# Performance work log

Measured on AMD Instinct MI355X. Metric: run time of the kernel, lower is better.

The kernel has to match this reference:

```python
import jax, jax.numpy as jnp
import numpy as np

D = 256       # dim
M = 50        # num_celltypes
NPATH = 65536 # path tokens (256*256)
N = M + NPATH
FF = 3        # focusing_factor
K = 5         # dwc kernel size


def find_closest_factors(num):
    for i in range(int(num ** 0.5), 0, -1):
        if num % i == 0:
            return (i, num // i)
    return (1, num)


def setup_inputs() -> dict:
    key = jax.random.key(0)
    ks = jax.random.split(key, 16)
    def w(k, shape, s=0.02):
        return jax.random.normal(k, shape, dtype=jnp.float32) * s
    z = lambda *s: jnp.zeros(s, jnp.float32)
    return {
        "x": jax.random.normal(ks[0], (1, N, D), dtype=jnp.float32),
        "W_qkv": w(ks[1], (D, 3 * D)),
        "scale_linear": w(ks[2], (1, 1, D)),
        "dwc_w": w(ks[3], (D, 1, K, K)),
        "dwc_b": w(ks[4], (D,)),
        "Wa": w(ks[5], (D, D)), "ba": z(D),
        "Wb": w(ks[6], (D, D)), "bb": z(D),
        "Wc": w(ks[7], (D, 1)), "bc": z(1),
        "W1": w(ks[8], (D, D)), "b1": z(D),
        "W2": w(ks[9], (D, D)), "b2": z(D),
        "W3a": w(ks[10], (2 * D, D)), "b3a": z(D),
        "W3b": w(ks[11], (D, D)), "b3b": z(D),
        "Wf": w(ks[12], (D, D)), "bf": z(D),
    }


def reference(x, W_qkv, scale_linear, dwc_w, dwc_b, Wa, ba, Wb, bb, Wc, bc,
              W1, b1, W2, b2, W3a, b3a, W3b, b3b, Wf, bf):
    scale = D ** -0.5
    qkv = x @ W_qkv                         # (1, N, 3D)
    q, k, v = jnp.split(qkv, 3, axis=-1)
    qc, qp = q[:, :M], q[:, M:]
    kc, kp = k[:, :M], k[:, M:]
    vc, vp = v[:, :M], v[:, M:]

    # --- softmax attention branches ---
    sa = jax.nn.softmax(jnp.einsum('bic,bjc->bij', qc * scale, kc), axis=-1)
    out_self_celltypes = sa @ vc            # (1, M, D)
    cap = jax.nn.softmax(jnp.einsum('bic,bjc->bij', qp * scale, kc), axis=-1)
    out_cross_path = cap @ vc               # (1, NPATH, D)
    cac = jax.nn.softmax(jnp.einsum('bic,bjc->bij', qc * scale, kp), axis=-1)
    out_cross_celltypes = cac @ vp          # (1, M, D)

    # --- focused linear attention on path tokens ---
    sp = jax.nn.softplus(scale_linear)
    ql = (jax.nn.relu(qp) + 1e-6) / sp
    kl = (jax.nn.relu(kp) + 1e-6) / sp
    qn = jnp.linalg.norm(ql, axis=-1, keepdims=True)
    kn = jnp.linalg.norm(kl, axis=-1, keepdims=True)
    ql = ql ** FF
    kl = kl ** FF
    ql = ql / jnp.linalg.norm(ql, axis=-1, keepdims=True) * qn
    kl = kl / jnp.linalg.norm(kl, axis=-1, keepdims=True) * kn
    zfac = 1.0 / (jnp.einsum('bic,bc->bi', ql, kl.sum(axis=1)) + 1e-6)
    kv = jnp.einsum('bjc,bjd->bcd', kl, vp)                 # (1, D, D)
    out_s = jnp.einsum('bic,bcd,bi->bid', ql, kv, zfac)     # (1, NPATH, D)

    # --- depthwise conv feature map ---
    wc, hc = find_closest_factors(NPATH)
    fm = vp.reshape(1, wc, hc, D).transpose(0, 3, 1, 2)     # b c w h
    fm = jax.lax.conv_general_dilated(
        fm, dwc_w, (1, 1), 'SAME',
        dimension_numbers=('NCHW', 'OIHW', 'NCHW'), feature_group_count=D)
    fm = fm + dwc_b[None, :, None, None]
    fm = fm.transpose(0, 2, 3, 1).reshape(1, NPATH, D)
    out_self_path = (out_s + fm) @ Wf + bf  # feamap_linear (dropout=eval)

    # --- gated attention net (shared weights, 4 calls) ---
    def gated(t):
        t = t[0]  # squeeze batch -> (n, D)
        a = jnp.tanh(t @ Wa + ba)
        g = jax.nn.sigmoid(t @ Wb + bb)
        return (a * g) @ Wc + bc  # (n, 1)

    A_cc = gated(out_cross_celltypes)
    A_cp = gated(out_cross_path)
    A_sc = gated(out_self_celltypes)
    A_sp = gated(out_self_path)

    # --- attention fusion (shared weights, 2 calls) ---
    def fuse(A1, A2, x1, x2):
        h1 = jax.nn.softmax(A1.T, axis=1) @ x1[0]   # (1, D)
        h1 = jax.nn.relu(h1 @ W1 + b1)
        h2 = jax.nn.softmax(A2.T, axis=1) @ x2[0]
        h2 = jax.nn.relu(h2 @ W2 + b2)
        f = jnp.concatenate([h1, h2], axis=1)       # (1, 2D)
        return jax.nn.relu(jax.nn.relu(f @ W3a + b3a) @ W3b + b3b)

    fusion_cross = fuse(A_cc, A_cp, out_cross_celltypes, out_cross_path)
    fusion_self = fuse(A_sc, A_sp, out_self_celltypes, out_self_path)
    return jnp.concatenate([fusion_cross, fusion_self], axis=1)  # (1, 2D)
```

## Files before the change

### kernel.cpp

```cpp
#include <hip/hip_runtime.h>
#include <hip/hip_bf16.h>
#include <math.h>


constexpr int DD = 256;
constexpr int MM = 50;
constexpr float SCL = 0.0625f;

constexpr size_t B_VPH = 0;
constexpr size_t B_QLH = (size_t)32 << 20;
constexpr size_t B_KLH = (size_t)64 << 20;
constexpr size_t B_E   = (size_t)96 << 20;
constexpr size_t B_SM  = (size_t)112 << 20;
constexpr size_t B_X   = B_SM + ((size_t)2 << 20);

constexpr size_t KLSUMR = 0;
constexpr size_t KLSUMP = 256;
constexpr size_t OCCDENP= 2304;
constexpr size_t W50P   = 2816;
constexpr size_t EDENP  = 3328;
constexpr size_t H2TP   = 3336;
constexpr size_t H2DENP = 5384;
constexpr size_t OCCRAW = 5392;
constexpr size_t ZEND   = 18192;
constexpr size_t QC     = ZEND;
constexpr size_t KC     = QC + 12800;
constexpr size_t VC     = KC + 12800;
constexpr size_t VCA    = VC + 12800;
constexpr size_t VCB    = VCA + 12800;
constexpr size_t WFA    = VCB + 12800;
constexpr size_t WFB    = WFA + 65536;
constexpr size_t BFA    = WFB + 65536;
constexpr size_t BFB    = BFA + 256;
constexpr size_t OSCB   = BFB + 256;
constexpr size_t OCCB   = OSCB + 12800;
constexpr size_t ASC    = OCCB + 12800;
constexpr size_t ACC50  = ASC + 64;
constexpr size_t SMEND  = ACC50 + 64;

constexpr size_t XT_WQKV = 0;
constexpr size_t XT_WFAT = 196608;
constexpr size_t XT_WFBT = 262144;
constexpr size_t XT_KVT  = 327680;
constexpr size_t XT_QCH  = 393216;
constexpr size_t XT_KCH  = 409600;
constexpr size_t XT_VCAT = 425984;
constexpr size_t XT_VCBT = 442368;
constexpr size_t XT_END  = 458752;
constexpr size_t WS_NEEDED = B_X + XT_END * 2;

typedef short bf16x8 __attribute__((ext_vector_type(8)));
typedef float f32x4 __attribute__((ext_vector_type(4)));

__device__ __forceinline__ float rcpf_(float x){ return __builtin_amdgcn_rcpf(x); }
__device__ __forceinline__ float fsig_(float x){ return rcpf_(1.0f + __expf(-x)); }
__device__ __forceinline__ float ftanh_(float x){ return 1.0f - 2.0f * rcpf_(__expf(2.0f * x) + 1.0f); }

__device__ __forceinline__ float bf2f(unsigned short u){
  return __uint_as_float(((unsigned int)u) << 16);
}
__device__ __forceinline__ unsigned short f2bf(float f){
  union { __hip_bfloat16 h; unsigned short u; } c;
  c.h = __float2bfloat16(f);
  return c.u;
}
__device__ __forceinline__ f32x4 mfma16(bf16x8 a, bf16x8 b, f32x4 c){
  return __builtin_amdgcn_mfma_f32_16x16x32_bf16(a, b, c, 0, 0, 0);
}

__device__ __forceinline__ float waveAllSum(float v){
  #pragma unroll
  for (int m = 1; m < 64; m <<= 1) v += __shfl_xor(v, m, 64);
  return v;
}

__device__ __forceinline__ size_t fragIdx(int n, int k, int K8){
  const int tile = n >> 4, cn = n & 15;
  const int k0 = k >> 5, kqi = (k >> 3) & 3, e = k & 7;
  return (((size_t)tile * K8 + k0) * 64 + (kqi * 16 + cn)) * 8 + e;
}

__device__ __forceinline__ int kvOff(int c, int k){
  return c * 40 + (c >> 3) * 8 + k;
}

__global__ void __launch_bounds__(256) k_prep0(const float* __restrict__ x, const float* __restrict__ Wqkv,
                                               float* qc, float* kc, float* vc,
                                               unsigned short* qch, unsigned short* kch,
                                               unsigned short* __restrict__ WT,
                                               const float* __restrict__ Wa, const float* __restrict__ Wb,
                                               const float* __restrict__ ba, const float* __restrict__ bb,
                                               const float* __restrict__ Wf, const float* __restrict__ bf,
                                               float* Wfa, float* Wfb, float* bfa, float* bfb,
                                               unsigned short* WfaTh, unsigned short* WfbTh){
  const int b = blockIdx.x, t = threadIdx.x;
  if (b < 48) {
    __shared__ unsigned short Tt[64][72];
    const int bn = b % 12, bk = b / 12;
    const int n0 = bn * 64, k0g = bk * 64;
    #pragma unroll
    for (int i = 0; i < 16; i++) {
      const int k_l = (t >> 6) + i * 4;
      const int n_l = t & 63;
      Tt[n_l][k_l] = f2bf(Wqkv[(size_t)(k0g + k_l) * 768 + n0 + n_l]);
    }
    __syncthreads();
    #pragma unroll
    for (int i = 0; i < 2; i++) {
      const int fr = t * 2 + i;
      const int t_l = fr >> 7;
      const int k0_l = (fr >> 6) & 1;
      const int lane_f = fr & 63;
      const int n_l = t_l * 16 + (lane_f & 15);
      const int k_l = k0_l * 32 + (lane_f >> 4) * 8;
      const int tg = (n0 >> 4) + t_l;
      const int k0gl = (k0g >> 5) + k0_l;
      bf16x8 v = *(const bf16x8*)&Tt[n_l][k_l];
      *(bf16x8*)&WT[(((size_t)tg * 8 + k0gl) * 64 + lane_f) * 8] = v;
    }
    return;
  }
  __shared__ float xs[256];
  const int j = t;
  if (b < 98) {
    const int r = b - 48;
    xs[j] = x[r * DD + j];
    __syncthreads();
    float aq = 0.f, ak = 0.f, av = 0.f;
    for (int k = 0; k < DD; k++) {
      float xv = xs[k];
      aq += xv * Wqkv[k * 768 + j];
      ak += xv * Wqkv[k * 768 + 256 + j];
      av += xv * Wqkv[k * 768 + 512 + j];
    }
    qc[r * DD + j] = aq; kc[r * DD + j] = ak; vc[r * DD + j] = av;
    qch[fragIdx(r, j, 8)] = f2bf(aq);
    kch[fragIdx(r, j, 8)] = f2bf(ak);
    if (r == 0) {
      for (int c = 50; c < 64; c++) {
        qch[fragIdx(c, j, 8)] = 0;
        kch[fragIdx(c, j, 8)] = 0;
      }
    }
    return;
  }
  const int bb2 = b - 98;
  const float* src; const float* Wm;
  if (bb2 < 256)      { src = Wf + bb2 * DD;         Wm = Wa; }
  else if (bb2 < 512) { src = Wf + (bb2 - 256) * DD; Wm = Wb; }
  else if (bb2 == 512){ src = bf;                    Wm = Wa; }
  else                { src = bf;                    Wm = Wb; }
  xs[j] = src[j];
  __syncthreads();
  float a = 0.f;
  for (int k = 0; k < DD; k++) a += xs[k] * Wm[k * DD + j];
  if (bb2 < 256)      { Wfa[bb2 * DD + j] = a; WfaTh[fragIdx(j, bb2, 8)] = f2bf(a); }
  else if (bb2 < 512) { Wfb[(bb2 - 256) * DD + j] = a; WfbTh[fragIdx(j, bb2 - 256, 8)] = f2bf(a); }
  else if (bb2 == 512) bfa[j] = a + ba[j];
  else bfb[j] = a + bb[j];
}

__global__ void __launch_bounds__(256) k_prep1(const float* vc, const float* Wa, const float* Wb,
                                               float* Vca, float* Vcb,
                                               unsigned short* VcaTh, unsigned short* VcbTh){
  __shared__ float rs[256];
  const int b = blockIdx.x, j = threadIdx.x;
  const int r = b;
  rs[j] = vc[r * DD + j];
  __syncthreads();
  float a = 0.f, bv = 0.f;
  for (int k = 0; k < DD; k++) { float v = rs[k]; a += v * Wa[k * DD + j]; bv += v * Wb[k * DD + j]; }
  Vca[r * DD + j] = a; Vcb[r * DD + j] = bv;
  VcaTh[fragIdx(j, r, 2)] = f2bf(a);
  VcbTh[fragIdx(j, r, 2)] = f2bf(bv);
  if (r == 0) {
    for (int c = 50; c < 64; c++) {
      VcaTh[fragIdx(j, c, 2)] = 0;
      VcbTh[fragIdx(j, c, 2)] = 0;
    }
  }
}

__global__ void __launch_bounds__(256) k_oscg(const float* __restrict__ qc, const float* __restrict__ kc,
                                              const float* __restrict__ vc,
                                              const float* __restrict__ Wa, const float* __restrict__ Wb,
                                              const float* __restrict__ ba, const float* __restrict__ bb,
                                              const float* __restrict__ Wc, const float* __restrict__ bc,
                                              float* __restrict__ osc, float* __restrict__ A){
  const int i = blockIdx.x, t = threadIdx.x;
  __shared__ float qs[256];
  __shared__ float P[64];
  __shared__ float red[4];
  qs[t] = qc[i * DD + t];
  __syncthreads();
  if (t < 64) {
    float s = -1e30f;
    if (t < 50) {
      float acc = 0.f;
      const float4* kr = (const float4*)&kc[t * DD];
      #pragma unroll 8
      for (int k = 0; k < 64; k++) {
        float4 kv = kr[k];
        float4 qv = *(const float4*)&qs[k * 4];
        acc += qv.x * kv.x + qv.y * kv.y + qv.z * kv.z + qv.w * kv.w;
      }
      s = acc * SCL;
    }
    float mx = s;
    #pragma unroll
    for (int m = 1; m < 64; m <<= 1) mx = fmaxf(mx, __shfl_xor(mx, m, 64));
    float e = (t < 50) ? __expf(s - mx) : 0.f;
    float den = waveAllSum(e);
    P[t] = e * rcpf_(den);
  }
  __syncthreads();
  float a = 0.f;
  for (int jj = 0; jj < 50; jj++) a += P[jj] * vc[jj * DD + t];
  osc[i * DD + t] = a;
  __syncthreads();
  qs[t] = a;
  __syncthreads();
  float u = 0.f, v = 0.f;
  for (int k = 0; k < DD; k++) { float tv = qs[k]; u += tv * Wa[k * DD + t]; v += tv * Wb[k * DD + t]; }
  float g = ftanh_(u + ba[t]) * fsig_(v + bb[t]) * Wc[t];
  g = waveAllSum(g);
  const int lane = t & 63, wv = t >> 6;
  if (lane == 0) red[wv] = g;
  __syncthreads();
  if (t == 0) A[i] = red[0] + red[1] + red[2] + red[3] + bc[0];
}

__global__ void __launch_bounds__(256) k_gated(const float* __restrict__ tin,
                                               const float* __restrict__ Wa, const float* __restrict__ Wb,
                                               const float* __restrict__ ba, const float* __restrict__ bb,
                                               const float* __restrict__ Wc, const float* __restrict__ bc,
                                               float* __restrict__ A){
  int r = blockIdx.x, j = threadIdx.x;
  __shared__ float ts[256];
  __shared__ float red[4];
  ts[j] = tin[r * DD + j];
  __syncthreads();
  float u = 0.f, v = 0.f;
  for (int k = 0; k < DD; k++) { float tv = ts[k]; u += tv * Wa[k * DD + j]; v += tv * Wb[k * DD + j]; }
  float g = ftanh_(u + ba[j]) * fsig_(v + bb[j]) * Wc[j];
  g = waveAllSum(g);
  int lane = j & 63, wv = j >> 6;
  if (lane == 0) red[wv] = g;
  __syncthreads();
  if (j == 0) A[r] = red[0] + red[1] + red[2] + red[3] + bc[0];
}

__global__ void __launch_bounds__(256) k_path1(
    const float* __restrict__ x, const unsigned short* __restrict__ WTf,
    const float* __restrict__ sln,
    const unsigned short* __restrict__ kchf, const unsigned short* __restrict__ qchf,
    const unsigned short* __restrict__ VcaTf, const unsigned short* __restrict__ VcbTf,
    const float* __restrict__ ba, const float* __restrict__ bb,
    const float* __restrict__ Wc, const float* __restrict__ bc,
    unsigned short* __restrict__ vph, unsigned short* __restrict__ qlh, unsigned short* __restrict__ klh,
    unsigned short* __restrict__ Eh, float* __restrict__ w50p, float* __restrict__ edenp, float* __restrict__ occdenp){
  __shared__ __align__(16) char arena[38912];
  unsigned short (*Psh)[72]   = (unsigned short (*)[72])arena;
  float (*denp)[4]            = (float (*)[4])(arena + 4608);
  unsigned short (*qpsb)[264] = (unsigned short (*)[264])(arena + 5120);
  unsigned short (*kpsb)[264] = (unsigned short (*)[264])(arena + 22016);

  const int tid = threadIdx.x;
  const int i0 = blockIdx.x * 32;
  const int part = blockIdx.x & 7;
  const int lane = tid & 63;
  const int wvv = tid >> 6;
  const int cn = lane & 15;
  const int m0 = (lane >> 4) * 4;
  const int kq = (lane >> 4) * 8;

  for (int l = tid; l < 2048; l += 256) {
    const int r = l >> 6, c4 = (l & 63) * 4;
    const float4 xv = *(const float4*)&x[(size_t)(MM + i0 + r) * DD + c4];
    ushort4 o; o.x = f2bf(xv.x); o.y = f2bf(xv.y); o.z = f2bf(xv.z); o.w = f2bf(xv.w);
    *(ushort4*)&qpsb[r][c4] = o;
  }
  __syncthreads();

  bf16x8 af0[8], af1[8];
  #pragma unroll
  for (int k0 = 0; k0 < 8; k0++) {
    af0[k0] = *(const bf16x8*)&qpsb[cn][k0 * 32 + kq];
    af1[k0] = *(const bf16x8*)&qpsb[16 + cn][k0 * 32 + kq];
  }
  __syncthreads();

  bf16x8 b0[8], b1[8];
  {
    const unsigned short* Bt = WTf + ((size_t)wvv * 8 * 64 + lane) * 8;
    #pragma unroll
    for (int k0 = 0; k0 < 8; k0++) b0[k0] = *(const bf16x8*)&Bt[(size_t)k0 * 512];
  }
  #pragma unroll 1
  for (int tt = 0; tt < 12; tt++) {
    const int t = wvv + 4 * tt;
    if (tt + 1 < 12) {
      const unsigned short* Bt = WTf + (((size_t)(t + 4) * 8) * 64 + lane) * 8;
      #pragma unroll
      for (int k0 = 0; k0 < 8; k0++) b1[k0] = *(const bf16x8*)&Bt[(size_t)k0 * 512];
    }
    f32x4 acc0 = {0.f, 0.f, 0.f, 0.f};
    f32x4 acc1 = {0.f, 0.f, 0.f, 0.f};
    #pragma unroll
    for (int k0 = 0; k0 < 8; k0++) {
      acc0 = mfma16(af0[k0], b0[k0], acc0);
      acc1 = mfma16(af1[k0], b0[k0], acc1);
    }
    if (t < 16) {
      int c = t * 16 + cn;
      #pragma unroll
      for (int i = 0; i < 4; i++) {
        qpsb[m0 + i][c] = f2bf(acc0[i]);
        qpsb[16 + m0 + i][c] = f2bf(acc1[i]);
      }
    } else if (t < 32) {
      int c = (t - 16) * 16 + cn;
      #pragma unroll
      for (int i = 0; i < 4; i++) {
        kpsb[m0 + i][c] = f2bf(acc0[i]);
        kpsb[16 + m0 + i][c] = f2bf(acc1[i]);
      }
    } else {
      int c = (t - 32) * 16 + cn;
      #pragma unroll
      for (int i = 0; i < 4; i++) {
        vph[(size_t)(i0 + m0 + i) * DD + c] = f2bf(acc0[i]);
        vph[(size_t)(i0 + 16 + m0 + i) * DD + c] = f2bf(acc1[i]);
      }
    }
    #pragma unroll
    for (int k0 = 0; k0 < 8; k0++) b0[k0] = b1[k0];
  }
  __syncthreads();

  float ep0[4], ep1[4];
  {
    f32x4 accp0 = {0.f,0.f,0.f,0.f}, accp1 = {0.f,0.f,0.f,0.f};
    f32x4 accc0 = {0.f,0.f,0.f,0.f}, accc1 = {0.f,0.f,0.f,0.f};
    const unsigned short* Bk = kchf + ((size_t)wvv * 8 * 64 + lane) * 8;
    const unsigned short* Bq = qchf + ((size_t)wvv * 8 * 64 + lane) * 8;
    #pragma unroll
    for (int k0 = 0; k0 < 8; k0++) {
      bf16x8 aq0 = *(const bf16x8*)&qpsb[cn][k0 * 32 + kq];
      bf16x8 aq1 = *(const bf16x8*)&qpsb[16 + cn][k0 * 32 + kq];
      bf16x8 ak0 = *(const bf16x8*)&kpsb[cn][k0 * 32 + kq];
      bf16x8 ak1 = *(const bf16x8*)&kpsb[16 + cn][k0 * 32 + kq];
      bf16x8 bk = *(const bf16x8*)&Bk[(size_t)k0 * 512];
      bf16x8 bq = *(const bf16x8*)&Bq[(size_t)k0 * 512];
      accp0 = mfma16(aq0, bk, accp0);
      accp1 = mfma16(aq1, bk, accp1);
      accc0 = mfma16(ak0, bq, accc0);
      accc1 = mfma16(ak1, bq, accc1);
    }
    const int col = wvv * 16 + cn;
    const bool ok = (col < 50);
    #pragma unroll
    for (int i = 0; i < 4; i++) {
      ep0[i] = ok ? __expf(accp0[i] * SCL) : 0.f;
      ep1[i] = ok ? __expf(accp1[i] * SCL) : 0.f;
    }
    float osum = 0.f;
    #pragma unroll
    for (int i = 0; i < 4; i++) {
      unsigned short h0 = ok ? f2bf(__expf(accc0[i] * SCL)) : (unsigned short)0;
      unsigned short h1 = ok ? f2bf(__expf(accc1[i] * SCL)) : (unsigned short)0;
      Eh[(size_t)(i0 + m0 + i) * 64 + col] = h0;
      Eh[(size_t)(i0 + 16 + m0 + i) * 64 + col] = h1;
      if (ok) osum += bf2f(h0) + bf2f(h1);
    }
    osum += __shfl_xor(osum, 16, 64);
    osum += __shfl_xor(osum, 32, 64);
    if (lane < 16 && ok) atomicAdd(&occdenp[part * 64 + col], osum);
    float d0[4], d1[4];
    #pragma unroll
    for (int i = 0; i < 4; i++) { d0[i] = ep0[i]; d1[i] = ep1[i]; }
    #pragma unroll
    for (int m = 1; m < 16; m <<= 1) {
      #pragma unroll
      for (int i = 0; i < 4; i++) {
        d0[i] += __shfl_xor(d0[i], m, 64);
        d1[i] += __shfl_xor(d1[i], m, 64);
      }
    }
    if (cn == 0) {
      #pragma unroll
      for (int i = 0; i < 4; i++) {
        denp[m0 + i][wvv] = d0[i];
        denp[16 + m0 + i][wvv] = d1[i];
      }
    }
  }
  __syncthreads();

  {
    const int col = wvv * 16 + cn;
    #pragma unroll
    for (int i = 0; i < 4; i++) {
      float4 dp = *(const float4*)&denp[m0 + i][0];
      Psh[m0 + i][col] = f2bf(ep0[i] * rcpf_(dp.x + dp.y + dp.z + dp.w));
      float4 dq = *(const float4*)&denp[16 + m0 + i][0];
      Psh[16 + m0 + i][col] = f2bf(ep1[i] * rcpf_(dq.x + dq.y + dq.z + dq.w));
    }
  }

  float4 sl4 = ((const float4*)sln)[lane];
  float4 rsp;
  rsp.x = rcpf_(log1pf(expf(sl4.x))); rsp.y = rcpf_(log1pf(expf(sl4.y)));
  rsp.z = rcpf_(log1pf(expf(sl4.z))); rsp.w = rcpf_(log1pf(expf(sl4.w)));
  float4 ba4 = ((const float4*)ba)[lane];
  float4 bb4 = ((const float4*)bb)[lane];
  float4 wc4 = ((const float4*)Wc)[lane];
  float bcv = bc[0];
  for (int rr = 0; rr < 8; rr++) {
    const int r = wvv * 8 + rr;
    const int row = i0 + r;
    ushort4 qu = *(const ushort4*)&qpsb[r][lane * 4];
    ushort4 ku = *(const ushort4*)&kpsb[r][lane * 4];
    float4 q4 = {bf2f(qu.x), bf2f(qu.y), bf2f(qu.z), bf2f(qu.w)};
    float4 k4 = {bf2f(ku.x), bf2f(ku.y), bf2f(ku.z), bf2f(ku.w)};
    float4 lq, lk;
    lq.x = (fmaxf(q4.x, 0.f) + 1e-6f) * rsp.x; lq.y = (fmaxf(q4.y, 0.f) + 1e-6f) * rsp.y;
    lq.z = (fmaxf(q4.z, 0.f) + 1e-6f) * rsp.z; lq.w = (fmaxf(q4.w, 0.f) + 1e-6f) * rsp.w;
    lk.x = (fmaxf(k4.x, 0.f) + 1e-6f) * rsp.x; lk.y = (fmaxf(k4.y, 0.f) + 1e-6f) * rsp.y;
    lk.z = (fmaxf(k4.z, 0.f) + 1e-6f) * rsp.z; lk.w = (fmaxf(k4.w, 0.f) + 1e-6f) * rsp.w;
    float4 q3, k3;
    q3.x = lq.x*lq.x*lq.x; q3.y = lq.y*lq.y*lq.y; q3.z = lq.z*lq.z*lq.z; q3.w = lq.w*lq.w*lq.w;
    k3.x = lk.x*lk.x*lk.x; k3.y = lk.y*lk.y*lk.y; k3.z = lk.z*lk.z*lk.z; k3.w = lk.w*lk.w*lk.w;
    float n1q = lq.x*lq.x + lq.y*lq.y + lq.z*lq.z + lq.w*lq.w;
    float n3q = q3.x*q3.x + q3.y*q3.y + q3.z*q3.z + q3.w*q3.w;
    float n1k = lk.x*lk.x + lk.y*lk.y + lk.z*lk.z + lk.w*lk.w;
    float n3k = k3.x*k3.x + k3.y*k3.y + k3.z*k3.z + k3.w*k3.w;
    n1q = waveAllSum(n1q); n3q = waveAllSum(n3q);
    n1k = waveAllSum(n1k); n3k = waveAllSum(n3k);
    float fq = sqrtf(n1q * rcpf_(n3q));
    float fk = sqrtf(n1k * rcpf_(n3k));
    ushort4 qo, ko;
    qo.x = f2bf(q3.x * fq); qo.y = f2bf(q3.y * fq); qo.z = f2bf(q3.z * fq); qo.w = f2bf(q3.w * fq);
    ko.x = f2bf(k3.x * fk); ko.y = f2bf(k3.y * fk); ko.z = f2bf(k3.z * fk); ko.w = f2bf(k3.w * fk);
    *(ushort4*)&qlh[(size_t)row * DD + lane * 4] = qo;
    *(ushort4*)&klh[(size_t)row * DD + lane * 4] = ko;
  }
  __syncthreads();

  {
    bf16x8 ap0[2], ap1[2];
    #pragma unroll
    for (int k0 = 0; k0 < 2; k0++) {
      ap0[k0] = *(const bf16x8*)&Psh[cn][k0 * 32 + kq];
      ap1[k0] = *(const bf16x8*)&Psh[16 + cn][k0 * 32 + kq];
    }
    #pragma unroll 1
    for (int tt = 0; tt < 4; tt++) {
      const int nt = wvv * 4 + tt;
      const unsigned short* Bu = VcaTf + (((size_t)nt * 2) * 64 + lane) * 8;
      const unsigned short* Bv = VcbTf + (((size_t)nt * 2) * 64 + lane) * 8;
      f32x4 au0 = {0.f,0.f,0.f,0.f}, au1 = {0.f,0.f,0.f,0.f};
      f32x4 av0 = {0.f,0.f,0.f,0.f}, av1 = {0.f,0.f,0.f,0.f};
      #pragma unroll
      for (int k0 = 0; k0 < 2; k0++) {
        bf16x8 bu = *(const bf16x8*)&Bu[(size_t)k0 * 512];
        bf16x8 bv = *(const bf16x8*)&Bv[(size_t)k0 * 512];
        au0 = mfma16(ap0[k0], bu, au0);
        au1 = mfma16(ap1[k0], bu, au1);
        av0 = mfma16(ap0[k0], bv, av0);
        av1 = mfma16(ap1[k0], bv, av1);
      }
      #pragma unroll
      for (int i = 0; i < 4; i++) {
        qpsb[m0 + i][nt * 16 + cn] = f2bf(au0[i]);
        qpsb[16 + m0 + i][nt * 16 + cn] = f2bf(au1[i]);
        kpsb[m0 + i][nt * 16 + cn] = f2bf(av0[i]);
        kpsb[16 + m0 + i][nt * 16 + cn] = f2bf(av1[i]);
      }
    }
  }
  __syncthreads();

  #pragma unroll
  for (int rr = 0; rr < 8; rr++) {
    const int r = wvv * 8 + rr;
    ushort4 uu = *(const ushort4*)&qpsb[r][lane * 4];
    ushort4 vv = *(const ushort4*)&kpsb[r][lane * 4];
    float g = ftanh_(bf2f(uu.x) + ba4.x) * fsig_(bf2f(vv.x) + bb4.x) * wc4.x
            + ftanh_(bf2f(uu.y) + ba4.y) * fsig_(bf2f(vv.y) + bb4.y) * wc4.y
            + ftanh_(bf2f(uu.z) + ba4.z) * fsig_(bf2f(vv.z) + bb4.z) * wc4.z
            + ftanh_(bf2f(uu.w) + ba4.w) * fsig_(bf2f(vv.w) + bb4.w) * wc4.w;
    g = waveAllSum(g);
    if (lane == 0) *(float*)&Psh[r][64] = __expf(g + bcv);
  }
  __syncthreads();
  if (tid < 64) {
    float s = 0.f;
    #pragma unroll
    for (int r = 0; r < 32; r++) s += *(const float*)&Psh[r][64] * bf2f(Psh[r][tid]);
    atomicAdd(&w50p[part * 64 + tid], s);
  }
  if (tid == 0) {
    float es = 0.f;
    #pragma unroll
    for (int r = 0; r < 32; r++) es += *(const float*)&Psh[r][64];
    atomicAdd(&edenp[part], es);
  }
}

__global__ void __launch_bounds__(256) k_occnum(const unsigned short* __restrict__ Eh,
                                                const unsigned short* __restrict__ vph,
                                                float* __restrict__ occraw){
  __shared__ __align__(16) unsigned short EhT[2608];
  __shared__ __align__(16) unsigned short BvpT[10480];
  const int tid = threadIdx.x;
  const int lane = tid & 63;
  const int wvv = tid >> 6;
  const int cn = lane & 15;
  const int m0 = (lane >> 4) * 4;
  const int kq = (lane >> 4) * 8;
  const int z  = blockIdx.x;
  const int jj = tid >> 3;
  const int c8 = (tid & 7) * 8;

  f32x4 acc[4][4];
  #pragma unroll
  for (int mt = 0; mt < 4; mt++)
    #pragma unroll
    for (int tl = 0; tl < 4; tl++) acc[mt][tl] = (f32x4){0.f,0.f,0.f,0.f};

  const int jbase = z * 512;
  #pragma unroll 1
  for (int step = 0; step < 16; step++) {
    const int j0 = jbase + step * 32;
    {
      bf16x8 av = *(const bf16x8*)&Eh[(size_t)(j0 + jj) * 64 + c8];
      #pragma unroll
      for (int i = 0; i < 8; i++) EhT[kvOff(c8 + i, jj)] = (unsigned short)av[i];
      #pragma unroll
      for (int rep = 0; rep < 4; rep++) {
        bf16x8 bv = *(const bf16x8*)&vph[(size_t)(j0 + jj) * 256 + rep * 64 + c8];
        #pragma unroll
        for (int i = 0; i < 8; i++) BvpT[kvOff(rep * 64 + c8 + i, jj)] = (unsigned short)bv[i];
      }
    }
    __syncthreads();
    bf16x8 afr[4], bfr[4];
    #pragma unroll
    for (int mt = 0; mt < 4; mt++)
      afr[mt] = *(const bf16x8*)&EhT[kvOff(cn + mt * 16, kq)];
    #pragma unroll
    for (int tl = 0; tl < 4; tl++)
      bfr[tl] = *(const bf16x8*)&BvpT[kvOff(wvv * 64 + tl * 16 + cn, kq)];
    #pragma unroll
    for (int mt = 0; mt < 4; mt++)
      #pragma unroll
      for (int tl = 0; tl < 4; tl++) acc[mt][tl] = mfma16(afr[mt], bfr[tl], acc[mt][tl]);
    __syncthreads();
  }
  #pragma unroll
  for (int mt = 0; mt < 4; mt++)
    #pragma unroll
    for (int i = 0; i < 4; i++) {
      const int ri = mt * 16 + m0 + i;
      if (ri < 50) {
        #pragma unroll
        for (int tl = 0; tl < 4; tl++) {
          const int d = wvv * 64 + tl * 16 + cn;
          atomicAdd(&occraw[ri * DD + d], acc[mt][tl][i]);
        }
      }
    }
}

__global__ void __launch_bounds__(256) k_kv(const unsigned short* __restrict__ klh,
                                            const unsigned short* __restrict__ vph,
                                            unsigned short* __restrict__ PP,
                                            float* __restrict__ klsump){
  __shared__ __align__(16) unsigned short AklT[2608];
  __shared__ __align__(16) unsigned short BvpT[10480];
  const int tid = threadIdx.x;
  const int lane = tid & 63;
  const int wvv = tid >> 6;
  const int cn = lane & 15;
  const int m0 = (lane >> 4) * 4;
  const int kq = (lane >> 4) * 8;
  const int cb = blockIdx.x;
  const int z  = blockIdx.y;
  const int jj = tid >> 3;
  const int c8 = (tid & 7) * 8;

  f32x4 acc[4][4];
  f32x4 acc1[4];
  #pragma unroll
  for (int mt = 0; mt < 4; mt++) {
    acc1[mt] = (f32x4){0.f,0.f,0.f,0.f};
    #pragma unroll
    for (int tl = 0; tl < 4; tl++) acc[mt][tl] = (f32x4){0.f,0.f,0.f,0.f};
  }
  bf16x8 ones;
  #pragma unroll
  for (int i = 0; i < 8; i++) ones[i] = (short)0x3F80;

  const int jbase = z * 512;
  #pragma unroll 1
  for (int step = 0; step < 16; step++) {
    const int j0 = jbase + step * 32;
    {
      bf16x8 av = *(const bf16x8*)&klh[(size_t)(j0 + jj) * 256 + cb * 64 + c8];
      #pragma unroll
      for (int i = 0; i < 8; i++) AklT[kvOff(c8 + i, jj)] = (unsigned short)av[i];
      #pragma unroll
      for (int rep = 0; rep < 4; rep++) {
        bf16x8 bv = *(const bf16x8*)&vph[(size_t)(j0 + jj) * 256 + rep * 64 + c8];
        #pragma unroll
        for (int i = 0; i < 8; i++) BvpT[kvOff(rep * 64 + c8 + i, jj)] = (unsigned short)bv[i];
      }
    }
    __syncthreads();
    bf16x8 afr[4], bfr[4];
    #pragma unroll
    for (int mt = 0; mt < 4; mt++)
      afr[mt] = *(const bf16x8*)&AklT[kvOff(cn + mt * 16, kq)];
    #pragma unroll
    for (int tl = 0; tl < 4; tl++)
      bfr[tl] = *(const bf16x8*)&BvpT[kvOff(wvv * 64 + tl * 16 + cn, kq)];
    #pragma unroll
    for (int mt = 0; mt < 4; mt++) {
      acc1[mt] = mfma16(afr[mt], ones, acc1[mt]);
      #pragma unroll
      for (int tl = 0; tl < 4; tl++) acc[mt][tl] = mfma16(afr[mt], bfr[tl], acc[mt][tl]);
    }
    __syncthreads();
  }
  unsigned short* P = PP + ((size_t)(cb * 128 + z)) * 16384;
  #pragma unroll
  for (int mt = 0; mt < 4; mt++)
    #pragma unroll
    for (int tl = 0; tl < 4; tl++) {
      const int n = (wvv * 4 + tl) * 16 + cn;
      #pragma unroll
      for (int i = 0; i < 4; i++)
        P[(size_t)(mt * 16 + m0 + i) * 256 + n] = f2bf(acc[mt][tl][i]);
    }
  if (wvv == 0 && cn == 0) {
    #pragma unroll
    for (int mt = 0; mt < 4; mt++)
      #pragma unroll
      for (int i = 0; i < 4; i++)
        atomicAdd(&klsump[(z & 7) * 256 + cb * 64 + mt * 16 + m0 + i], acc1[mt][i]);
  }
}

__global__ void __launch_bounds__(256) k_fin2(const unsigned short* __restrict__ PP,
                                              unsigned short* __restrict__ kvTf,
                                              const float* __restrict__ occraw,
                                              const float* __restrict__ occdenp,
                                              float* __restrict__ occ,
                                              const float* __restrict__ klsump,
                                              float* __restrict__ klsum){
  const int b = blockIdx.x, d = threadIdx.x;
  if (b < 256) {
    const int cb = b >> 6, m = b & 63;
    float s = 0.f;
    for (int z = 0; z < 128; z++)
      s += bf2f(PP[((size_t)(cb * 128 + z)) * 16384 + (size_t)m * 256 + d]);
    kvTf[fragIdx(d, b, 8)] = f2bf(s);
  } else if (b < 306) {
    const int i = b - 256;
    float den = 0.f;
    #pragma unroll
    for (int p = 0; p < 8; p++) den += occdenp[p * 64 + i];
    occ[i * DD + d] = occraw[i * DD + d] / den;
  } else {
    float s = 0.f;
    #pragma unroll
    for (int p = 0; p < 8; p++) s += klsump[p * 256 + d];
    klsum[d] = s;
  }
}

__global__ void __launch_bounds__(256) k_tail(const unsigned short* __restrict__ qlh,
                                              const unsigned short* __restrict__ kvTf,
                                              const float* __restrict__ klsum,
                                              const unsigned short* __restrict__ vph,
                                              const float* __restrict__ dwcw, const float* __restrict__ dwcb,
                                              const unsigned short* __restrict__ WfaTf,
                                              const unsigned short* __restrict__ WfbTf,
                                              const float* __restrict__ bfa, const float* __restrict__ bfb,
                                              const float* __restrict__ Wc, const float* __restrict__ bc,
                                              float* __restrict__ h2tp, float* __restrict__ h2denp){
  __shared__ unsigned short Tsh[32][264];
  __shared__ unsigned short OSb[32][264];
  __shared__ unsigned short aVb[32][264];
  __shared__ float zf[32];
  __shared__ float ev[32];
  const int tid = threadIdx.x;
  const int i0 = blockIdx.x * 32;
  const int part = blockIdx.x & 7;
  const int lane = tid & 63;
  const int wvv = tid >> 6;
  const int cn = lane & 15;
  const int m0 = (lane >> 4) * 4;
  const int kq = (lane >> 4) * 8;
  for (int l = tid; l < 2048; l += 256) {
    int r = l >> 6, c4 = (l & 63) * 4;
    *(ushort4*)&Tsh[r][c4] = *(const ushort4*)&qlh[(size_t)(i0 + r) * DD + c4];
  }
  __syncthreads();
  {
    bf16x8 afq0[8], afq1[8];
    #pragma unroll
    for (int k0 = 0; k0 < 8; k0++) {
      afq0[k0] = *(const bf16x8*)&Tsh[cn][k0 * 32 + kq];
      afq1[k0] = *(const bf16x8*)&Tsh[16 + cn][k0 * 32 + kq];
    }
    #pragma unroll 1
    for (int tt = 0; tt < 4; tt++) {
      const int nt = wvv * 4 + tt;
      const unsigned short* Bt = kvTf + (((size_t)nt * 8) * 64 + lane) * 8;
      f32x4 acc0 = {0.f,0.f,0.f,0.f};
      f32x4 acc1 = {0.f,0.f,0.f,0.f};
      #pragma unroll
      for (int k0 = 0; k0 < 8; k0++) {
        bf16x8 b = *(const bf16x8*)&Bt[(size_t)k0 * 512];
        acc0 = mfma16(afq0[k0], b, acc0);
        acc1 = mfma16(afq1[k0], b, acc1);
      }
      #pragma unroll
      for (int i = 0; i < 4; i++) {
        OSb[m0 + i][nt * 16 + cn] = f2bf(acc0[i]);
        OSb[16 + m0 + i][nt * 16 + cn] = f2bf(acc1[i]);
      }
    }
  }
  {
    float4 ks4 = ((const float4*)klsum)[lane];
    #pragma unroll
    for (int rr = 0; rr < 8; rr++) {
      const int r = wvv * 8 + rr;
      ushort4 q4 = *(const ushort4*)&Tsh[r][lane * 4];
      float s = bf2f(q4.x)*ks4.x + bf2f(q4.y)*ks4.y + bf2f(q4.z)*ks4.z + bf2f(q4.w)*ks4.w;
      s = waveAllSum(s);
      if (lane == 0) zf[r] = rcpf_(s + 1e-6f);
    }
  }
  __syncthreads();
  const int j = tid;
  float w[25];
  #pragma unroll
  for (int t = 0; t < 25; t++) w[t] = dwcw[j * 25 + t];
  const float bias = dwcb[j];
  const int y = i0 >> 8, x0 = i0 & 255;
  float fm[32];
  #pragma unroll
  for (int r = 0; r < 32; r++) fm[r] = bias;
  #pragma unroll
  for (int dy = -2; dy <= 2; dy++) {
    const int yy = y + dy;
    if ((unsigned)yy > 255u) continue;
    float buf[36];
    #pragma unroll
    for (int i = 0; i < 36; i++) {
      const int xx = x0 - 2 + i;
      buf[i] = ((unsigned)xx <= 255u) ? bf2f(vph[(size_t)((yy << 8) + xx) * DD + j]) : 0.f;
    }
    const float* wr = &w[(dy + 2) * 5];
    #pragma unroll
    for (int r = 0; r < 32; r++)
      fm[r] += buf[r] * wr[0] + buf[r+1] * wr[1] + buf[r+2] * wr[2]
             + buf[r+3] * wr[3] + buf[r+4] * wr[4];
  }
  #pragma unroll
  for (int r = 0; r < 32; r++) {
    fm[r] = bf2f(OSb[r][j]) * zf[r] + fm[r];
    Tsh[r][j] = f2bf(fm[r]);
  }
  __syncthreads();
  {
    bf16x8 aft0[8], aft1[8];
    #pragma unroll
    for (int k0 = 0; k0 < 8; k0++) {
      aft0[k0] = *(const bf16x8*)&Tsh[cn][k0 * 32 + kq];
      aft1[k0] = *(const bf16x8*)&Tsh[16 + cn][k0 * 32 + kq];
    }
    #pragma unroll 1
    for (int jb = 0; jb < 8; jb++) {
      const int nt = wvv * 4 + (jb & 3);
      const unsigned short* Bt = ((jb < 4) ? WfaTf : WfbTf) + (((size_t)nt * 8) * 64 + lane) * 8;
      f32x4 acc0 = {0.f,0.f,0.f,0.f};
      f32x4 acc1 = {0.f,0.f,0.f,0.f};
      #pragma unroll
      for (int k0 = 0; k0 < 8; k0++) {
        bf16x8 b = *(const bf16x8*)&Bt[(size_t)k0 * 512];
        acc0 = mfma16(aft0[k0], b, acc0);
        acc1 = mfma16(aft1[k0], b, acc1);
      }
      unsigned short (*dst)[264] = (jb < 4) ? OSb : aVb;
      #pragma unroll
      for (int i = 0; i < 4; i++) {
        dst[m0 + i][nt * 16 + cn] = f2bf(acc0[i]);
        dst[16 + m0 + i][nt * 16 + cn] = f2bf(acc1[i]);
      }
    }
  }
  __syncthreads();
  {
    float4 bfa4 = ((const float4*)bfa)[lane];
    float4 bfb4 = ((const float4*)bfb)[lane];
    float4 wc4 = ((const float4*)Wc)[lane];
    const float bcv = bc[0];
    #pragma unroll
    for (int rr = 0; rr < 8; rr++) {
      const int r = wvv * 8 + rr;
      ushort4 uu = *(const ushort4*)&OSb[r][lane * 4];
      ushort4 vv = *(const ushort4*)&aVb[r][lane * 4];
      float g = ftanh_(bf2f(uu.x) + bfa4.x) * fsig_(bf2f(vv.x) + bfb4.x) * wc4.x
              + ftanh_(bf2f(uu.y) + bfa4.y) * fsig_(bf2f(vv.y) + bfb4.y) * wc4.y
              + ftanh_(bf2f(uu.z) + bfa4.z) * fsig_(bf2f(vv.z) + bfb4.z) * wc4.z
              + ftanh_(bf2f(uu.w) + bfa4.w) * fsig_(bf2f(vv.w) + bfb4.w) * wc4.w;
      g = waveAllSum(g);
      if (lane == 0) ev[r] = __expf(g + bcv);
    }
  }
  __syncthreads();
  float hp = 0.f;
  #pragma unroll
  for (int r = 0; r < 32; r++) hp += ev[r] * fm[r];
  atomicAdd(&h2tp[part * 256 + j], hp);
  if (tid == 0) {
    float es = 0.f;
    #pragma unroll
    for (int r = 0; r < 32; r++) es += ev[r];
    atomicAdd(&h2denp[part], es);
  }
}

__global__ void __launch_bounds__(256) k_final(
    const float* __restrict__ A_cc, const float* __restrict__ occ,
    const float* __restrict__ A_sc, const float* __restrict__ osc,
    const float* __restrict__ w50p, const float* __restrict__ edenp,
    const float* __restrict__ h2tp, const float* __restrict__ h2denp,
    const float* __restrict__ vc, const float* __restrict__ Wf, const float* __restrict__ bf,
    const float* __restrict__ W1, const float* __restrict__ b1,
    const float* __restrict__ W2, const float* __restrict__ b2,
    const float* __restrict__ W3a, const float* __restrict__ b3a,
    const float* __restrict__ W3b, const float* __restrict__ b3b,
    float* __restrict__ out){
  int j = threadIdx.x;
  __shared__ float pw[64];
  __shared__ float w50t[64];
  __shared__ float t1[256], t2[256], h1[256], h2[256], fz[512], z1[256];
  if (j < 64) {
    float s = 0.f;
    #pragma unroll
    for (int p = 0; p < 8; p++) s += w50p[p * 64 + j];
    w50t[j] = s;
  }
  float edentot = 0.f, h2dentot = 0.f;
  #pragma unroll
  for (int p = 0; p < 8; p++) { edentot += edenp[p]; h2dentot += h2denp[p]; }
  if (j < 64) pw[j] = (j < 50) ? expf(A_cc[j]) : 0.f;
  __syncthreads();
  float den = 0.f;
  for (int i = 0; i < 50; i++) den += pw[i];
  float raw = 0.f;
  for (int i = 0; i < 50; i++) raw += pw[i] * occ[i * DD + j];
  t1[j] = raw / den;
  float r2 = 0.f;
  for (int i = 0; i < 50; i++) r2 += w50t[i] * vc[i * DD + j];
  t2[j] = r2 / edentot;
  __syncthreads();
  float a1 = 0.f, a2 = 0.f;
  for (int k = 0; k < DD; k++) { a1 += t1[k] * W1[k * DD + j]; a2 += t2[k] * W2[k * DD + j]; }
  h1[j] = fmaxf(a1 + b1[j], 0.f);
  h2[j] = fmaxf(a2 + b2[j], 0.f);
  __syncthreads();
  fz[j] = h1[j]; fz[256 + j] = h2[j];
  __syncthreads();
  float z = 0.f;
  for (int k = 0; k < 512; k++) z += fz[k] * W3a[k * DD + j];
  z1[j] = fmaxf(z + b3a[j], 0.f);
  __syncthreads();
  float o = 0.f;
  for (int k = 0; k < DD; k++) o += z1[k] * W3b[k * DD + j];
  out[j] = fmaxf(o + b3b[j], 0.f);
  __syncthreads();
  if (j < 64) pw[j] = (j < 50) ? expf(A_sc[j]) : 0.f;
  __syncthreads();
  den = 0.f;
  for (int i = 0; i < 50; i++) den += pw[i];
  raw = 0.f;
  for (int i = 0; i < 50; i++) raw += pw[i] * osc[i * DD + j];
  t1[j] = raw / den;
  {
    float s = 0.f;
    #pragma unroll
    for (int p = 0; p < 8; p++) s += h2tp[p * 256 + j];
    t2[j] = s / h2dentot;
  }
  __syncthreads();
  float hs = 0.f;
  for (int k = 0; k < DD; k++) hs += t2[k] * Wf[k * DD + j];
  __syncthreads();
  t2[j] = hs + bf[j];
  __syncthreads();
  a1 = 0.f; a2 = 0.f;
  for (int k = 0; k < DD; k++) { a1 += t1[k] * W1[k * DD + j]; a2 += t2[k] * W2[k * DD + j]; }
  h1[j] = fmaxf(a1 + b1[j], 0.f);
  h2[j] = fmaxf(a2 + b2[j], 0.f);
  __syncthreads();
  fz[j] = h1[j]; fz[256 + j] = h2[j];
  __syncthreads();
  z = 0.f;
  for (int k = 0; k < 512; k++) z += fz[k] * W3a[k * DD + j];
  z1[j] = fmaxf(z + b3a[j], 0.f);
  __syncthreads();
  o = 0.f;
  for (int k = 0; k < DD; k++) o += z1[k] * W3b[k * DD + j];
  out[256 + j] = fmaxf(o + b3b[j], 0.f);
}

extern "C" void kernel_launch(void* const* d_in, const int* in_sizes, int n_in,
                              void* d_out, int out_size, void* d_ws, size_t ws_size,
                              hipStream_t stream) {
  if (ws_size < WS_NEEDED) return;
  const float* x   = (const float*)d_in[0];
  const float* Wqkv= (const float*)d_in[1];
  const float* sln = (const float*)d_in[2];
  const float* dwcw= (const float*)d_in[3];
  const float* dwcb= (const float*)d_in[4];
  const float* Wa  = (const float*)d_in[5];
  const float* ba  = (const float*)d_in[6];
  const float* Wb  = (const float*)d_in[7];
  const float* bb  = (const float*)d_in[8];
  const float* Wc  = (const float*)d_in[9];
  const float* bc  = (const float*)d_in[10];
  const float* W1  = (const float*)d_in[11];
  const float* b1  = (const float*)d_in[12];
  const float* W2  = (const float*)d_in[13];
  const float* b2  = (const float*)d_in[14];
  const float* W3a = (const float*)d_in[15];
  const float* b3a = (const float*)d_in[16];
  const float* W3b = (const float*)d_in[17];
  const float* b3b = (const float*)d_in[18];
  const float* Wf  = (const float*)d_in[19];
  const float* bf  = (const float*)d_in[20];

  char* wsb = (char*)d_ws;
  unsigned short* VPH = (unsigned short*)(wsb + B_VPH);
  unsigned short* QLH = (unsigned short*)(wsb + B_QLH);
  unsigned short* KLH = (unsigned short*)(wsb + B_KLH);
  unsigned short* EHB = (unsigned short*)(wsb + B_E);
  float* SM = (float*)(wsb + B_SM);
  unsigned short* XT = (unsigned short*)(wsb + B_X);
  float* outp = (float*)d_out;

  hipMemsetAsync((void*)SM, 0, ZEND * sizeof(float), stream);

  k_prep0<<<612, 256, 0, stream>>>(x, Wqkv, SM + QC, SM + KC, SM + VC,
                                   XT + XT_QCH, XT + XT_KCH, XT + XT_WQKV,
                                   Wa, Wb, ba, bb, Wf, bf,
                                   SM + WFA, SM + WFB, SM + BFA, SM + BFB,
                                   XT + XT_WFAT, XT + XT_WFBT);
  k_prep1<<<50, 256, 0, stream>>>(SM + VC, Wa, Wb,
                                  SM + VCA, SM + VCB, XT + XT_VCAT, XT + XT_VCBT);
  k_oscg<<<50, 256, 0, stream>>>(SM + QC, SM + KC, SM + VC, Wa, Wb, ba, bb, Wc, bc,
                                 SM + OSCB, SM + ASC);

  k_path1<<<2048, 256, 0, stream>>>(x, XT + XT_WQKV, sln, XT + XT_KCH, XT + XT_QCH,
                                    XT + XT_VCAT, XT + XT_VCBT, ba, bb, Wc, bc,
                                    VPH, QLH, KLH, EHB, SM + W50P, SM + EDENP, SM + OCCDENP);
  k_occnum<<<128, 256, 0, stream>>>(EHB, VPH, SM + OCCRAW);
  k_kv<<<dim3(4, 128), 256, 0, stream>>>(KLH, VPH, EHB, SM + KLSUMP);
  k_fin2<<<307, 256, 0, stream>>>(EHB, XT + XT_KVT,
                                  SM + OCCRAW, SM + OCCDENP, SM + OCCB,
                                  SM + KLSUMP, SM + KLSUMR);
  k_gated<<<50, 256, 0, stream>>>(SM + OCCB, Wa, Wb, ba, bb, Wc, bc, SM + ACC50);

  k_tail<<<2048, 256, 0, stream>>>(QLH, XT + XT_KVT, SM + KLSUMR, VPH, dwcw, dwcb,
                                   XT + XT_WFAT, XT + XT_WFBT, SM + BFA, SM + BFB,
                                   Wc, bc, SM + H2TP, SM + H2DENP);

  k_final<<<1, 256, 0, stream>>>(SM + ACC50, SM + OCCB, SM + ASC, SM + OSCB,
                                 SM + W50P, SM + EDENP, SM + H2TP, SM + H2DENP,
                                 SM + VC, Wf, bf, W1, b1, W2, b2, W3a, b3a, W3b, b3b, outp);
}
```

Baseline: 528.4 us.

## Fold occupancy numerator into k_kv, merge gated net into fin2, halve partials

The separate k_occnum kernel becomes a fifth column-block of k_kv, since both stream vph against a 64-wide A operand. Each block now covers 1024 rows instead of 512, which halves the number of partial KV products. k_gated is folded into k_fin2, and the partial reduction is vectorized to 8 bf16 per load. Together this removes two kernel launches and halves partial-buffer traffic, at the cost of fewer blocks (320 instead of 512+128) and a longer serial loop per block. PP now lives at an offset inside the E buffer so it no longer overwrites Eh, which the occupancy block still reads.

```diff
diff --git a/kernel.cpp b/kernel.cpp
--- a/kernel.cpp
+++ b/kernel.cpp
@@ -13,6 +13,8 @@
 constexpr size_t B_E   = (size_t)96 << 20;
 constexpr size_t B_SM  = (size_t)112 << 20;
 constexpr size_t B_X   = B_SM + ((size_t)2 << 20);
+
+constexpr size_t PP_OFF = (size_t)4 << 20;
 
 constexpr size_t KLSUMR = 0;
 constexpr size_t KLSUMP = 256;
@@ -228,26 +230,6 @@
   if (lane == 0) red[wv] = g;
   __syncthreads();
   if (t == 0) A[i] = red[0] + red[1] + red[2] + red[3] + bc[0];
-}
-
-__global__ void __launch_bounds__(256) k_gated(const float* __restrict__ tin,
-                                               const float* __restrict__ Wa, const float* __restrict__ Wb,
-                                               const float* __restrict__ ba, const float* __restrict__ bb,
-                                               const float* __restrict__ Wc, const float* __restrict__ bc,
-                                               float* __restrict__ A){
-  int r = blockIdx.x, j = threadIdx.x;
-  __shared__ float ts[256];
-  __shared__ float red[4];
-  ts[j] = tin[r * DD + j];
-  __syncthreads();
-  float u = 0.f, v = 0.f;
-  for (int k = 0; k < DD; k++) { float tv = ts[k]; u += tv * Wa[k * DD + j]; v += tv * Wb[k * DD + j]; }
-  float g = ftanh_(u + ba[j]) * fsig_(v + bb[j]) * Wc[j];
-  g = waveAllSum(g);
-  int lane = j & 63, wv = j >> 6;
-  if (lane == 0) red[wv] = g;
-  __syncthreads();
-  if (j == 0) A[r] = red[0] + red[1] + red[2] + red[3] + bc[0];
 }
 
 __global__ void __launch_bounds__(256) k_path1(
@@ -508,76 +490,13 @@
   }
 }
 
-__global__ void __launch_bounds__(256) k_occnum(const unsigned short* __restrict__ Eh,
-                                                const unsigned short* __restrict__ vph,
-                                                float* __restrict__ occraw){
-  __shared__ __align__(16) unsigned short EhT[2608];
-  __shared__ __align__(16) unsigned short BvpT[10480];
-  const int tid = threadIdx.x;
-  const int lane = tid & 63;
-  const int wvv = tid >> 6;
-  const int cn = lane & 15;
-  const int m0 = (lane >> 4) * 4;
-  const int kq = (lane >> 4) * 8;
-  const int z  = blockIdx.x;
-  const int jj = tid >> 3;
-  const int c8 = (tid & 7) * 8;
-
-  f32x4 acc[4][4];
-  #pragma unroll
-  for (int mt = 0; mt < 4; mt++)
-    #pragma unroll
-    for (int tl = 0; tl < 4; tl++) acc[mt][tl] = (f32x4){0.f,0.f,0.f,0.f};
-
-  const int jbase = z * 512;
-  #pragma unroll 1
-  for (int step = 0; step < 16; step++) {
-    const int j0 = jbase + step * 32;
-    {
-      bf16x8 av = *(const bf16x8*)&Eh[(size_t)(j0 + jj) * 64 + c8];
-      #pragma unroll
-      for (int i = 0; i < 8; i++) EhT[kvOff(c8 + i, jj)] = (unsigned short)av[i];
-      #pragma unroll
-      for (int rep = 0; rep < 4; rep++) {
-        bf16x8 bv = *(const bf16x8*)&vph[(size_t)(j0 + jj) * 256 + rep * 64 + c8];
-        #pragma unroll
-        for (int i = 0; i < 8; i++) BvpT[kvOff(rep * 64 + c8 + i, jj)] = (unsigned short)bv[i];
-      }
-    }
-    __syncthreads();
-    bf16x8 afr[4], bfr[4];
-    #pragma unroll
-    for (int mt = 0; mt < 4; mt++)
-      afr[mt] = *(const bf16x8*)&EhT[kvOff(cn + mt * 16, kq)];
-    #pragma unroll
-    for (int tl = 0; tl < 4; tl++)
-      bfr[tl] = *(const bf16x8*)&BvpT[kvOff(wvv * 64 + tl * 16 + cn, kq)];
-    #pragma unroll
-    for (int mt = 0; mt < 4; mt++)
-      #pragma unroll
-      for (int tl = 0; tl < 4; tl++) acc[mt][tl] = mfma16(afr[mt], bfr[tl], acc[mt][tl]);
-    __syncthreads();
-  }
-  #pragma unroll
-  for (int mt = 0; mt < 4; mt++)
-    #pragma unroll
-    for (int i = 0; i < 4; i++) {
-      const int ri = mt * 16 + m0 + i;
-      if (ri < 50) {
-        #pragma unroll
-        for (int tl = 0; tl < 4; tl++) {
-          const int d = wvv * 64 + tl * 16 + cn;
-          atomicAdd(&occraw[ri * DD + d], acc[mt][tl][i]);
-        }
-      }
-    }
-}
-
 __global__ void __launch_bounds__(256) k_kv(const unsigned short* __restrict__ klh,
+                                            const unsigned short* __restrict__ Eh,
                                             const unsigned short* __restrict__ vph,
                                             unsigned short* __restrict__ PP,
-                                            float* __restrict__ klsump){
-  __shared__ __align__(16) unsigned short AklT[2608];
+                                            float* __restrict__ klsump,
+                                            float* __restrict__ occraw){
+  __shared__ __align__(16) unsigned short AT[2608];
   __shared__ __align__(16) unsigned short BvpT[10480];
   const int tid = threadIdx.x;
   const int lane = tid & 63;
@@ -589,6 +508,7 @@
   const int z  = blockIdx.y;
   const int jj = tid >> 3;
   const int c8 = (tid & 7) * 8;
+  const bool isOcc = (cb == 4);
 
   f32x4 acc[4][4];
   f32x4 acc1[4];
@@ -602,14 +522,16 @@
   #pragma unroll
   for (int i = 0; i < 8; i++) ones[i] = (short)0x3F80;
 
-  const int jbase = z * 512;
+  const int jbase = z * 1024;
   #pragma unroll 1
-  for (int step = 0; step < 16; step++) {
+  for (int step = 0; step < 32; step++) {
     const int j0 = jbase + step * 32;
     {
-      bf16x8 av = *(const bf16x8*)&klh[(size_t)(j0 + jj) * 256 + cb * 64 + c8];
-      #pragma unroll
-      for (int i = 0; i < 8; i++) AklT[kvOff(c8 + i, jj)] = (unsigned short)av[i];
+      bf16x8 av;
+      if (isOcc) av = *(const bf16x8*)&Eh[(size_t)(j0 + jj) * 64 + c8];
+      else       av = *(const bf16x8*)&klh[(size_t)(j0 + jj) * 256 + cb * 64 + c8];
+      #pragma unroll
+      for (int i = 0; i < 8; i++) AT[kvOff(c8 + i, jj)] = (unsigned short)av[i];
       #pragma unroll
       for (int rep = 0; rep < 4; rep++) {
         bf16x8 bv = *(const bf16x8*)&vph[(size_t)(j0 + jj) * 256 + rep * 64 + c8];
@@ -621,19 +543,37 @@
     bf16x8 afr[4], bfr[4];
     #pragma unroll
     for (int mt = 0; mt < 4; mt++)
-      afr[mt] = *(const bf16x8*)&AklT[kvOff(cn + mt * 16, kq)];
+      afr[mt] = *(const bf16x8*)&AT[kvOff(cn + mt * 16, kq)];
     #pragma unroll
     for (int tl = 0; tl < 4; tl++)
       bfr[tl] = *(const bf16x8*)&BvpT[kvOff(wvv * 64 + tl * 16 + cn, kq)];
-    #pragma unroll
-    for (int mt = 0; mt < 4; mt++) {
-      acc1[mt] = mfma16(afr[mt], ones, acc1[mt]);
+    if (!isOcc) {
+      #pragma unroll
+      for (int mt = 0; mt < 4; mt++) acc1[mt] = mfma16(afr[mt], ones, acc1[mt]);
+    }
+    #pragma unroll
+    for (int mt = 0; mt < 4; mt++)
       #pragma unroll
       for (int tl = 0; tl < 4; tl++) acc[mt][tl] = mfma16(afr[mt], bfr[tl], acc[mt][tl]);
-    }
     __syncthreads();
   }
-  unsigned short* P = PP + ((size_t)(cb * 128 + z)) * 16384;
+  if (isOcc) {
+    #pragma unroll
+    for (int mt = 0; mt < 4; mt++)
+      #pragma unroll
+      for (int i = 0; i < 4; i++) {
+        const int ri = mt * 16 + m0 + i;
+        if (ri < 50) {
+          #pragma unroll
+          for (int tl = 0; tl < 4; tl++) {
+            const int d = wvv * 64 + tl * 16 + cn;
+            atomicAdd(&occraw[ri * DD + d], acc[mt][tl][i]);
+          }
+        }
+      }
+    return;
+  }
+  unsigned short* P = PP + ((size_t)(cb * 64 + z)) * 16384;
   #pragma unroll
   for (int mt = 0; mt < 4; mt++)
     #pragma unroll
@@ -658,21 +598,48 @@
                                               const float* __restrict__ occdenp,
                                               float* __restrict__ occ,
                                               const float* __restrict__ klsump,
-                                              float* __restrict__ klsum){
-  const int b = blockIdx.x, d = threadIdx.x;
-  if (b < 256) {
-    const int cb = b >> 6, m = b & 63;
-    float s = 0.f;
-    for (int z = 0; z < 128; z++)
-      s += bf2f(PP[((size_t)(cb * 128 + z)) * 16384 + (size_t)m * 256 + d]);
-    kvTf[fragIdx(d, b, 8)] = f2bf(s);
-  } else if (b < 306) {
-    const int i = b - 256;
+                                              float* __restrict__ klsum,
+                                              const float* __restrict__ Wa, const float* __restrict__ Wb,
+                                              const float* __restrict__ ba, const float* __restrict__ bb,
+                                              const float* __restrict__ Wc, const float* __restrict__ bc,
+                                              float* __restrict__ A){
+  __shared__ float ts[256];
+  __shared__ float red[4];
+  const int b = blockIdx.x, tid = threadIdx.x;
+  if (b < 32) {
+    const int gm = b * 8 + (tid >> 5);
+    const int cb = gm >> 6, m = gm & 63;
+    const int d8 = (tid & 31) * 8;
+    float s[8];
+    #pragma unroll
+    for (int e = 0; e < 8; e++) s[e] = 0.f;
+    for (int z = 0; z < 64; z++) {
+      bf16x8 v = *(const bf16x8*)&PP[((size_t)(cb * 64 + z)) * 16384 + (size_t)m * 256 + d8];
+      #pragma unroll
+      for (int e = 0; e < 8; e++) s[e] += bf2f((unsigned short)v[e]);
+    }
+    #pragma unroll
+    for (int e = 0; e < 8; e++)
+      kvTf[fragIdx(d8 + e, gm, 8)] = f2bf(s[e]);
+  } else if (b < 82) {
+    const int i = b - 32, j = tid;
     float den = 0.f;
     #pragma unroll
     for (int p = 0; p < 8; p++) den += occdenp[p * 64 + i];
-    occ[i * DD + d] = occraw[i * DD + d] / den;
+    float t = occraw[i * DD + j] / den;
+    occ[i * DD + j] = t;
+    ts[j] = t;
+    __syncthreads();
+    float u = 0.f, v = 0.f;
+    for (int k = 0; k < DD; k++) { float tv = ts[k]; u += tv * Wa[k * DD + j]; v += tv * Wb[k * DD + j]; }
+    float g = ftanh_(u + ba[j]) * fsig_(v + bb[j]) * Wc[j];
+    g = waveAllSum(g);
+    const int lane = j & 63, wv = j >> 6;
+    if (lane == 0) red[wv] = g;
+    __syncthreads();
+    if (j == 0) A[i] = red[0] + red[1] + red[2] + red[3] + bc[0];
   } else {
+    const int d = tid;
     float s = 0.f;
     #pragma unroll
     for (int p = 0; p < 8; p++) s += klsump[p * 256 + d];
@@ -952,6 +919,7 @@
   unsigned short* QLH = (unsigned short*)(wsb + B_QLH);
   unsigned short* KLH = (unsigned short*)(wsb + B_KLH);
   unsigned short* EHB = (unsigned short*)(wsb + B_E);
+  unsigned short* PPB = EHB + PP_OFF;
   float* SM = (float*)(wsb + B_SM);
   unsigned short* XT = (unsigned short*)(wsb + B_X);
   float* outp = (float*)d_out;
@@ -971,12 +939,11 @@
   k_path1<<<2048, 256, 0, stream>>>(x, XT + XT_WQKV, sln, XT + XT_KCH, XT + XT_QCH,
                                     XT + XT_VCAT, XT + XT_VCBT, ba, bb, Wc, bc,
                                     VPH, QLH, KLH, EHB, SM + W50P, SM + EDENP, SM + OCCDENP);
-  k_occnum<<<128, 256, 0, stream>>>(EHB, VPH, SM + OCCRAW);
-  k_kv<<<dim3(4, 128), 256, 0, stream>>>(KLH, VPH, EHB, SM + KLSUMP);
-  k_fin2<<<307, 256, 0, stream>>>(EHB, XT + XT_KVT,
-                                  SM + OCCRAW, SM + OCCDENP, SM + OCCB,
-                                  SM + KLSUMP, SM + KLSUMR);
-  k_gated<<<50, 256, 0, stream>>>(SM + OCCB, Wa, Wb, ba, bb, Wc, bc, SM + ACC50);
+  k_kv<<<dim3(5, 64), 256, 0, stream>>>(KLH, EHB, VPH, PPB, SM + KLSUMP, SM + OCCRAW);
+  k_fin2<<<83, 256, 0, stream>>>(PPB, XT + XT_KVT,
+                                 SM + OCCRAW, SM + OCCDENP, SM + OCCB,
+                                 SM + KLSUMP, SM + KLSUMR,
+                                 Wa, Wb, ba, bb, Wc, bc, SM + ACC50);
 
   k_tail<<<2048, 256, 0, stream>>>(QLH, XT + XT_KVT, SM + KLSUMR, VPH, dwcw, dwcb,
                                    XT + XT_WFAT, XT + XT_WFBT, SM + BFA, SM + BFB,
```

Result: faster. 512.8 us (-3.0%).
